# Performance work log

Hardware: AMD Instinct MI355X
Metric: run time of the kernel (lower is better)

## Reference

```python
import jax, jax.numpy as jnp
import numpy as np

NL, D, H, MLP, P, HW, L, KEEP = 6, 1024, 16, 4096, 16, 14, 196, 98
DH = D // H


def layer_norm(x, s, b):
    m = jnp.mean(x, axis=-1, keepdims=True)
    v = jnp.mean(jnp.square(x - m), axis=-1, keepdims=True)
    return (x - m) * jax.lax.rsqrt(v + 1e-6) * s + b


def gather_by_einsum(x, ids):
    # faithful to FLIP: one-hot gather expressed as matmul (sharding-friendly)
    mat = jax.nn.one_hot(ids, x.shape[1], dtype=x.dtype)
    return jnp.einsum('nl...,nkl->nk...', x, mat)


def setup_inputs():
    key = jax.random.key(0)
    ks = jax.random.split(key, 10)
    s = 0.02
    return {
        'imgs': jax.random.normal(ks[0], (32, 224, 224, 3), jnp.float32),
        'noise': jax.random.uniform(ks[1], (32, L), jnp.float32),
        'patch_w': jax.random.normal(ks[2], (P * P * 3, D), jnp.float32) * s,
        'patch_b': jnp.zeros((D,), jnp.float32),
        'pos_emb': jax.random.normal(ks[3], (1, L, D), jnp.float32) * s,
        'cls_token': jnp.zeros((1, 1, D), jnp.float32),
        'ln1_s': jnp.ones((NL, D), jnp.float32),
        'ln1_b': jnp.zeros((NL, D), jnp.float32),
        'wq': jax.random.normal(ks[4], (NL, D, D), jnp.float32) * s,
        'bq': jnp.zeros((NL, D), jnp.float32),
        'wk': jax.random.normal(ks[5], (NL, D, D), jnp.float32) * s,
        'bk': jnp.zeros((NL, D), jnp.float32),
        'wv': jax.random.normal(ks[6], (NL, D, D), jnp.float32) * s,
        'bv': jnp.zeros((NL, D), jnp.float32),
        'wo': jax.random.normal(ks[7], (NL, D, D), jnp.float32) * s,
        'bo': jnp.zeros((NL, D), jnp.float32),
        'ln2_s': jnp.ones((NL, D), jnp.float32),
        'ln2_b': jnp.zeros((NL, D), jnp.float32),
        'w1': jax.random.normal(ks[8], (NL, D, MLP), jnp.float32) * s,
        'b1': jnp.zeros((NL, MLP), jnp.float32),
        'w2': jax.random.normal(ks[9], (NL, MLP, D), jnp.float32) * s,
        'b2': jnp.zeros((NL, D), jnp.float32),
        'lnf_s': jnp.ones((D,), jnp.float32),
        'lnf_b': jnp.zeros((D,), jnp.float32),
    }


def reference(imgs, noise, patch_w, patch_b, pos_emb, cls_token,
              ln1_s, ln1_b, wq, bq, wk, bk, wv, bv, wo, bo,
              ln2_s, ln2_b, w1, b1, w2, b2, lnf_s, lnf_b):
    N = imgs.shape[0]
    # patchify: (N,224,224,3) -> (N, L=196, 768); stride-16 conv == patch matmul
    x = imgs.reshape(N, HW, P, HW, P, 3).transpose(0, 1, 3, 2, 4, 5).reshape(N, L, P * P * 3)
    x = x @ patch_w + patch_b          # (N, L, D)
    x = x + pos_emb

    # random_mask (mask_ratio=0.5 -> keep 98 of 196 tokens)
    ids_shuffle = jnp.argsort(noise, axis=1)
    ids_restore = jnp.argsort(ids_shuffle, axis=1)
    ids_keep = ids_shuffle[:, :KEEP]
    x = gather_by_einsum(x, ids_keep)  # (N, KEEP, D)
    mask = jnp.ones((N, L), x.dtype).at[:, :KEEP].set(0.0)
    mask = gather_by_einsum(mask, ids_restore)  # (N, L)

    # prepend cls token -> (N, 1+KEEP, D)
    x = jnp.concatenate([jnp.tile(cls_token, (N, 1, 1)), x], axis=1)

    scale = 1.0 / np.sqrt(DH).astype(np.float32)
    S = x.shape[1]
    for i in range(NL):
        y = layer_norm(x, ln1_s[i], ln1_b[i])
        q = (y @ wq[i] + bq[i]).reshape(N, S, H, DH)
        k = (y @ wk[i] + bk[i]).reshape(N, S, H, DH)
        v = (y @ wv[i] + bv[i]).reshape(N, S, H, DH)
        att = jax.nn.softmax(jnp.einsum('nqhd,nkhd->nhqk', q, k) * scale, axis=-1)
        o = jnp.einsum('nhqk,nkhd->nqhd', att, v).reshape(N, S, D)
        x = x + o @ wo[i] + bo[i]
        y = layer_norm(x, ln2_s[i], ln2_b[i])
        y = jax.nn.gelu(y @ w1[i] + b1[i]) @ w2[i] + b2[i]
        x = x + y
    x = layer_norm(x, lnf_s, lnf_b)
    return x, mask
```

## Files before the change

kernel.cpp:

```cpp
#include <hip/hip_runtime.h>
#include <hip/hip_bf16.h>
#include <math.h>

#define NLAYERS 6
#define DMODEL  1024
#define NHEADS  16
#define DHEAD   64
#define DMLP    4096
#define PSZ     16
#define HWN     14
#define LTOK    196
#define NKEEP   98
#define NIMG    32
#define SEQ     99
#define NS      (NIMG * SEQ)
#define NP      (NIMG * LTOK)
#define PDIM    768
#define QS      3072
#define SPAD    112
#define VT_PITCH 136
#define P_PITCH  136

typedef __attribute__((ext_vector_type(8))) short short8;
typedef __attribute__((ext_vector_type(4))) float f32x4;

__device__ __forceinline__ void gload16(const void* g, void* l) {
    __builtin_amdgcn_global_load_lds(
        (const __attribute__((address_space(1))) void*)g,
        (__attribute__((address_space(3))) void*)l, 16, 0, 0);
}

__global__ __launch_bounds__(256) void conv_transpose(
    const float* __restrict__ W, __hip_bfloat16* __restrict__ Wt, int K, int N,
    size_t src_zs, size_t dst_zs)
{
    __shared__ float tile[32][33];
    W += (size_t)blockIdx.z * src_zs;
    Wt += (size_t)blockIdx.z * dst_zs;
    int n0 = blockIdx.x * 32, k0 = blockIdx.y * 32;
    int tx = threadIdx.x & 31, ty = threadIdx.x >> 5;
#pragma unroll
    for (int i = 0; i < 4; ++i)
        tile[ty + i * 8][tx] = W[(size_t)(k0 + ty + i * 8) * N + n0 + tx];
    __syncthreads();
#pragma unroll
    for (int i = 0; i < 4; ++i)
        Wt[(size_t)(n0 + ty + i * 8) * K + k0 + tx] = __float2bfloat16(tile[tx][ty + i * 8]);
}

__global__ __launch_bounds__(256) void concat_bias(
    const float* __restrict__ bq, const float* __restrict__ bk,
    const float* __restrict__ bv, float* __restrict__ bqkv)
{
    int L = blockIdx.y;
    int i = blockIdx.x * 256 + threadIdx.x;
    float v;
    if (i < DMODEL)            v = bq[L * DMODEL + i];
    else if (i < 2 * DMODEL)   v = bk[L * DMODEL + i - DMODEL];
    else                       v = bv[L * DMODEL + i - 2 * DMODEL];
    bqkv[(size_t)L * QS + i] = v;
}

__global__ __launch_bounds__(256) void sort_kernel(
    const float* __restrict__ noise, int* __restrict__ ids_keep, float* __restrict__ mask)
{
    int n = blockIdx.x, tid = threadIdx.x;
    __shared__ float nz[LTOK];
    if (tid < LTOK) nz[tid] = noise[n * LTOK + tid];
    __syncthreads();
    if (tid < LTOK) {
        float val = nz[tid];
        int rank = 0;
        for (int j = 0; j < LTOK; ++j) {
            float vj = nz[j];
            rank += (vj < val) || (vj == val && j < tid);
        }
        mask[n * LTOK + tid] = (rank < NKEEP) ? 0.0f : 1.0f;
        if (rank < NKEEP) ids_keep[n * NKEEP + rank] = tid;
    }
}

__global__ __launch_bounds__(256) void patchify(
    const float* __restrict__ imgs, __hip_bfloat16* __restrict__ Ap)
{
    int row = blockIdx.x, tid = threadIdx.x;
    int n = row / LTOK, l = row % LTOK;
    int hy = l / HWN, hx = l % HWN;
    int py = tid >> 4, px = tid & 15;
    const float* src = imgs + (((size_t)(n * 224 + hy * 16 + py)) * 224 + hx * 16 + px) * 3;
    __hip_bfloat16* dst = Ap + (size_t)row * PDIM + tid * 3;
    dst[0] = __float2bfloat16(src[0]);
    dst[1] = __float2bfloat16(src[1]);
    dst[2] = __float2bfloat16(src[2]);
}

__global__ __launch_bounds__(256) void gather_cls(
    const float* __restrict__ x0, const float* __restrict__ cls,
    const int* __restrict__ ids_keep, float* __restrict__ x)
{
    int row = blockIdx.x, tid = threadIdx.x;
    int n = row / SEQ, s = row % SEQ;
    const float* src = (s == 0) ? cls
        : x0 + ((size_t)n * LTOK + ids_keep[n * NKEEP + (s - 1)]) * DMODEL;
    reinterpret_cast<float4*>(x + (size_t)row * DMODEL)[tid] =
        reinterpret_cast<const float4*>(src)[tid];
}

template <int OUTMODE>
__global__ __launch_bounds__(256) void ln_kernel(
    const float* __restrict__ x, const float* __restrict__ s, const float* __restrict__ b,
    float* __restrict__ of, __hip_bfloat16* __restrict__ ob)
{
    int row = blockIdx.x, tid = threadIdx.x;
    int lane = tid & 63, wid = tid >> 6;
    float4 t = reinterpret_cast<const float4*>(x + (size_t)row * DMODEL)[tid];
    float sum = t.x + t.y + t.z + t.w;
    float sq  = t.x * t.x + t.y * t.y + t.z * t.z + t.w * t.w;
#pragma unroll
    for (int m = 1; m < 64; m <<= 1) { sum += __shfl_xor(sum, m); sq += __shfl_xor(sq, m); }
    __shared__ float sm[8];
    if (lane == 0) { sm[wid] = sum; sm[4 + wid] = sq; }
    __syncthreads();
    sum = sm[0] + sm[1] + sm[2] + sm[3];
    sq  = sm[4] + sm[5] + sm[6] + sm[7];
    float mean = sum * (1.0f / DMODEL);
    float var  = sq * (1.0f / DMODEL) - mean * mean;
    float rstd = rsqrtf(var + 1e-6f);
    float4 sv = reinterpret_cast<const float4*>(s)[tid];
    float4 bv = reinterpret_cast<const float4*>(b)[tid];
    float o0 = (t.x - mean) * rstd * sv.x + bv.x;
    float o1 = (t.y - mean) * rstd * sv.y + bv.y;
    float o2 = (t.z - mean) * rstd * sv.z + bv.z;
    float o3 = (t.w - mean) * rstd * sv.w + bv.w;
    if (OUTMODE == 0) {
        reinterpret_cast<float4*>(of + (size_t)row * DMODEL)[tid] = make_float4(o0, o1, o2, o3);
    } else {
        __hip_bfloat16* p = ob + (size_t)row * DMODEL + tid * 4;
        p[0] = __float2bfloat16(o0); p[1] = __float2bfloat16(o1);
        p[2] = __float2bfloat16(o2); p[3] = __float2bfloat16(o3);
    }
}

template <int MODE>
__global__ __launch_bounds__(256) void gemm_mfma(
    const __hip_bfloat16* __restrict__ A, const __hip_bfloat16* __restrict__ Wt,
    const float* __restrict__ bias, const float* __restrict__ pos,
    float* __restrict__ Cf, __hip_bfloat16* __restrict__ Cb,
    int M, int N, int K)
{
    __shared__ __hip_bfloat16 As[2][128 * 32];
    __shared__ __hip_bfloat16 Bs[2][128 * 32];

    int tid = threadIdx.x;
    int lane = tid & 63, wid = tid >> 6;
    int quad = lane >> 4, l16 = lane & 15;
    int wm = wid & 1, wn = wid >> 1;
    int bm = blockIdx.x * 128, bn = blockIdx.y * 128;
    int Kc = K / gridDim.z;
    int koff = blockIdx.z * Kc;

    int rowA0 = tid >> 2,        rowA1 = (tid + 256) >> 2;
    int kcA0 = (tid & 3) ^ ((tid >> 3) & 3);
    int kcA1 = (tid & 3) ^ (((tid + 256) >> 3) & 3);
    int arow0 = bm + rowA0; if (arow0 >= M) arow0 = M - 1;
    int arow1 = bm + rowA1; if (arow1 >= M) arow1 = M - 1;
    const short* Ag0 = reinterpret_cast<const short*>(A) + (size_t)arow0 * K + koff + kcA0 * 8;
    const short* Ag1 = reinterpret_cast<const short*>(A) + (size_t)arow1 * K + koff + kcA1 * 8;
    const short* Bg0 = reinterpret_cast<const short*>(Wt) + (size_t)(bn + rowA0) * K + koff + kcA0 * 8;
    const short* Bg1 = reinterpret_cast<const short*>(Wt) + (size_t)(bn + rowA1) * K + koff + kcA1 * 8;

    int aOff[4], bOff[4];
#pragma unroll
    for (int t = 0; t < 4; ++t) {
        int row = wm * 64 + t * 16 + l16;
        aOff[t] = row * 64 + (quad ^ ((row >> 1) & 3)) * 16;
        int col = wn * 64 + t * 16 + l16;
        bOff[t] = col * 64 + (quad ^ ((col >> 1) & 3)) * 16;
    }

    f32x4 acc[4][4];
#pragma unroll
    for (int t = 0; t < 4; ++t)
#pragma unroll
        for (int u = 0; u < 4; ++u) { f32x4 z = {0.f, 0.f, 0.f, 0.f}; acc[t][u] = z; }

    auto stage = [&](int buf, int k0) {
        char* ad = (char*)As[buf];
        char* bd = (char*)Bs[buf];
        gload16(Ag0 + k0, ad + tid * 16);
        gload16(Ag1 + k0, ad + (tid + 256) * 16);
        gload16(Bg0 + k0, bd + tid * 16);
        gload16(Bg1 + k0, bd + (tid + 256) * 16);
    };
    auto compute = [&](int buf) {
        const char* ab = (const char*)As[buf];
        const char* bb = (const char*)Bs[buf];
        short8 a[4], b[4];
#pragma unroll
        for (int t = 0; t < 4; ++t) a[t] = *reinterpret_cast<const short8*>(ab + aOff[t]);
#pragma unroll
        for (int u = 0; u < 4; ++u) b[u] = *reinterpret_cast<const short8*>(bb + bOff[u]);
#pragma unroll
        for (int t = 0; t < 4; ++t)
#pragma unroll
            for (int u = 0; u < 4; ++u)
                acc[t][u] = __builtin_amdgcn_mfma_f32_16x16x32_bf16(a[t], b[u], acc[t][u], 0, 0, 0);
    };

    stage(0, 0);
    __syncthreads();
    for (int k0 = 0; k0 < Kc; k0 += 64) {
        stage(1, k0 + 32);
        compute(0);
        __syncthreads();
        if (k0 + 64 < Kc) stage(0, k0 + 64);
        compute(1);
        __syncthreads();
    }

    bool addb = (bias != nullptr) && (blockIdx.z == 0);
#pragma unroll
    for (int t = 0; t < 4; ++t) {
#pragma unroll
        for (int u = 0; u < 4; ++u) {
            int col = bn + wn * 64 + u * 16 + l16;
            float bcol = addb ? bias[col] : 0.0f;
#pragma unroll
            for (int i = 0; i < 4; ++i) {
                int row = bm + wm * 64 + t * 16 + quad * 4 + i;
                if (row >= M) continue;
                float val = acc[t][u][i] + bcol;
                size_t idx = (size_t)row * N + col;
                if (MODE == 0) {
                    if (pos) val += pos[(size_t)(row % LTOK) * N + col];
                    Cf[idx] = val;
                } else if (MODE == 1) {
                    atomicAdd(&Cf[idx], val);
                } else if (MODE == 2) {
                    float u3 = val * val * val;
                    float g = 0.5f * val *
                        (1.0f + tanhf(0.7978845608028654f * (val + 0.044715f * u3)));
                    Cb[idx] = __float2bfloat16(g);
                } else {
                    Cb[idx] = __float2bfloat16(val);
                }
            }
        }
    }
}

__global__ __launch_bounds__(256) void attn_mfma(
    const __hip_bfloat16* __restrict__ qkv, __hip_bfloat16* __restrict__ o)
{
    int n = blockIdx.x >> 4, h = blockIdx.x & 15;
    int tid = threadIdx.x, lane = tid & 63, wid = tid >> 6;
    int quad = lane >> 4, l16 = lane & 15;

    __shared__ __hip_bfloat16 Vt[DHEAD * VT_PITCH];
    __shared__ __hip_bfloat16 Ps[4][16 * P_PITCH];

    {
        int4 zz = make_int4(0, 0, 0, 0);
        int4* v4 = (int4*)Vt;
        int4* p4 = (int4*)Ps;
        for (int i = tid; i < (DHEAD * VT_PITCH) / 8; i += 256) v4[i] = zz;
        for (int i = tid; i < (4 * 16 * P_PITCH) / 8; i += 256) p4[i] = zz;
    }
    __syncthreads();
    for (int idx = tid; idx < SEQ * DHEAD; idx += 256) {
        int s = idx >> 6, d = idx & 63;
        Vt[d * VT_PITCH + s] = qkv[((size_t)(n * SEQ + s)) * QS + 2 * DMODEL + h * DHEAD + d];
    }
    __syncthreads();

    const short* qbase = reinterpret_cast<const short*>(qkv) + (size_t)n * SEQ * QS + h * DHEAD;
    const short* kbase = qbase + DMODEL;
    const float scale = 0.125f;

    for (int qt = wid; qt < 7; qt += 4) {
        int q0 = qt * 16;
        int qrow = q0 + l16; if (qrow >= SEQ) qrow = SEQ - 1;
        const short* qp = qbase + (size_t)qrow * QS + quad * 8;
        short8 aq0 = *reinterpret_cast<const short8*>(qp);
        short8 aq1 = *reinterpret_cast<const short8*>(qp + 32);

        f32x4 sc[7];
#pragma unroll
        for (int u = 0; u < 7; ++u) {
            int krow = u * 16 + l16; if (krow >= SEQ) krow = SEQ - 1;
            const short* kp = kbase + (size_t)krow * QS + quad * 8;
            short8 kb0 = *reinterpret_cast<const short8*>(kp);
            short8 kb1 = *reinterpret_cast<const short8*>(kp + 32);
            f32x4 s = {0.f, 0.f, 0.f, 0.f};
            s = __builtin_amdgcn_mfma_f32_16x16x32_bf16(aq0, kb0, s, 0, 0, 0);
            s = __builtin_amdgcn_mfma_f32_16x16x32_bf16(aq1, kb1, s, 0, 0, 0);
            sc[u] = s;
        }
#pragma unroll
        for (int u = 0; u < 7; ++u)
#pragma unroll
            for (int i = 0; i < 4; ++i)
                sc[u][i] *= scale;
        if (l16 >= 3) {
#pragma unroll
            for (int i = 0; i < 4; ++i) sc[6][i] = -1e30f;
        }
#pragma unroll
        for (int i = 0; i < 4; ++i) {
            float m = sc[0][i];
#pragma unroll
            for (int u = 1; u < 7; ++u) m = fmaxf(m, sc[u][i]);
            m = fmaxf(m, __shfl_xor(m, 1));
            m = fmaxf(m, __shfl_xor(m, 2));
            m = fmaxf(m, __shfl_xor(m, 4));
            m = fmaxf(m, __shfl_xor(m, 8));
            float sum = 0.f;
#pragma unroll
            for (int u = 0; u < 7; ++u) {
                float e = __expf(sc[u][i] - m);
                sc[u][i] = e;
                sum += e;
            }
            sum += __shfl_xor(sum, 1);
            sum += __shfl_xor(sum, 2);
            sum += __shfl_xor(sum, 4);
            sum += __shfl_xor(sum, 8);
            float inv = 1.0f / sum;
            __hip_bfloat16* pr = &Ps[wid][(quad * 4 + i) * P_PITCH];
#pragma unroll
            for (int u = 0; u < 7; ++u)
                pr[u * 16 + l16] = __float2bfloat16(sc[u][i] * inv);
        }
        short8 ap[4];
#pragma unroll
        for (int kc = 0; kc < 4; ++kc)
            ap[kc] = *reinterpret_cast<const short8*>(&Ps[wid][l16 * P_PITCH + kc * 32 + quad * 8]);
        f32x4 oacc[4];
#pragma unroll
        for (int dt = 0; dt < 4; ++dt) { f32x4 z = {0.f, 0.f, 0.f, 0.f}; oacc[dt] = z; }
#pragma unroll
        for (int kc = 0; kc < 4; ++kc) {
#pragma unroll
            for (int dt = 0; dt < 4; ++dt) {
                short8 vb = *reinterpret_cast<const short8*>(
                    &Vt[(dt * 16 + l16) * VT_PITCH + kc * 32 + quad * 8]);
                oacc[dt] = __builtin_amdgcn_mfma_f32_16x16x32_bf16(ap[kc], vb, oacc[dt], 0, 0, 0);
            }
        }
#pragma unroll
        for (int dt = 0; dt < 4; ++dt) {
#pragma unroll
            for (int i = 0; i < 4; ++i) {
                int row = q0 + quad * 4 + i;
                if (row < SEQ)
                    o[((size_t)(n * SEQ + row)) * DMODEL + h * DHEAD + dt * 16 + l16] =
                        __float2bfloat16(oacc[dt][i]);
            }
        }
    }
}

extern "C" void kernel_launch(void* const* d_in, const int* in_sizes, int n_in,
                              void* d_out, int out_size, void* d_ws, size_t ws_size,
                              hipStream_t stream)
{
    (void)in_sizes; (void)n_in; (void)out_size; (void)ws_size;
    const float* imgs    = (const float*)d_in[0];
    const float* noise   = (const float*)d_in[1];
    const float* patch_w = (const float*)d_in[2];
    const float* patch_b = (const float*)d_in[3];
    const float* pos_emb = (const float*)d_in[4];
    const float* cls     = (const float*)d_in[5];
    const float* ln1_s   = (const float*)d_in[6];
    const float* ln1_b   = (const float*)d_in[7];
    const float* wq      = (const float*)d_in[8];
    const float* bq      = (const float*)d_in[9];
    const float* wk      = (const float*)d_in[10];
    const float* bk      = (const float*)d_in[11];
    const float* wv      = (const float*)d_in[12];
    const float* bv      = (const float*)d_in[13];
    const float* wo      = (const float*)d_in[14];
    const float* bo      = (const float*)d_in[15];
    const float* ln2_s   = (const float*)d_in[16];
    const float* ln2_b   = (const float*)d_in[17];
    const float* w1      = (const float*)d_in[18];
    const float* b1      = (const float*)d_in[19];
    const float* w2      = (const float*)d_in[20];
    const float* b2      = (const float*)d_in[21];
    const float* lnf_s   = (const float*)d_in[22];
    const float* lnf_b   = (const float*)d_in[23];

    float* out_x    = (float*)d_out;
    float* out_mask = out_x + (size_t)NS * DMODEL;

    char* p = (char*)d_ws;
    auto alloc = [&](size_t bytes) {
        char* r = p; p += (bytes + 255) & ~(size_t)255; return r;
    };
    __hip_bfloat16* patch_wt = (__hip_bfloat16*)alloc((size_t)DMODEL * PDIM * 2);
    __hip_bfloat16* wqkvt    = (__hip_bfloat16*)alloc((size_t)NLAYERS * QS * DMODEL * 2);
    __hip_bfloat16* wot = (__hip_bfloat16*)alloc((size_t)NLAYERS * DMODEL * DMODEL * 2);
    __hip_bfloat16* w1t = (__hip_bfloat16*)alloc((size_t)NLAYERS * DMODEL * DMLP * 2);
    __hip_bfloat16* w2t = (__hip_bfloat16*)alloc((size_t)NLAYERS * DMODEL * DMLP * 2);
    float* bqkv     = (float*)alloc((size_t)NLAYERS * QS * 4);
    int*   ids_keep = (int*)alloc((size_t)NIMG * NKEEP * 4);
    float* x        = (float*)alloc((size_t)NS * DMODEL * 4);
    char* scratch = p;
    __hip_bfloat16* ybf  = (__hip_bfloat16*)alloc((size_t)NS * DMODEL * 2);
    __hip_bfloat16* qkv  = (__hip_bfloat16*)alloc((size_t)NS * QS * 2);
    __hip_bfloat16* obf  = (__hip_bfloat16*)alloc((size_t)NS * DMODEL * 2);
    __hip_bfloat16* h1bf = (__hip_bfloat16*)alloc((size_t)NS * DMLP * 2);
    __hip_bfloat16* Apatch = (__hip_bfloat16*)scratch;
    float* x0 = (float*)(scratch + (((size_t)NP * PDIM * 2 + 255) & ~(size_t)255));

    const size_t DD = (size_t)DMODEL * DMODEL;
    const size_t DM = (size_t)DMODEL * DMLP;

    conv_transpose<<<dim3(DMODEL / 32, PDIM / 32, 1), 256, 0, stream>>>(
        patch_w, patch_wt, PDIM, DMODEL, PDIM * DMODEL, PDIM * DMODEL);
    conv_transpose<<<dim3(DMODEL / 32, DMODEL / 32, NLAYERS), 256, 0, stream>>>(
        wq, wqkvt, DMODEL, DMODEL, DD, (size_t)QS * DMODEL);
    conv_transpose<<<dim3(DMODEL / 32, DMODEL / 32, NLAYERS), 256, 0, stream>>>(
        wk, wqkvt + DD, DMODEL, DMODEL, DD, (size_t)QS * DMODEL);
    conv_transpose<<<dim3(DMODEL / 32, DMODEL / 32, NLAYERS), 256, 0, stream>>>(
        wv, wqkvt + 2 * DD, DMODEL, DMODEL, DD, (size_t)QS * DMODEL);
    conv_transpose<<<dim3(DMODEL / 32, DMODEL / 32, NLAYERS), 256, 0, stream>>>(
        wo, wot, DMODEL, DMODEL, DD, DD);
    conv_transpose<<<dim3(DMLP / 32, DMODEL / 32, NLAYERS), 256, 0, stream>>>(
        w1, w1t, DMODEL, DMLP, DM, DM);
    conv_transpose<<<dim3(DMODEL / 32, DMLP / 32, NLAYERS), 256, 0, stream>>>(
        w2, w2t, DMLP, DMODEL, DM, DM);
    concat_bias<<<dim3(QS / 256, NLAYERS), 256, 0, stream>>>(bq, bk, bv, bqkv);

    sort_kernel<<<NIMG, 256, 0, stream>>>(noise, ids_keep, out_mask);
    patchify<<<NP, 256, 0, stream>>>(imgs, Apatch);
    gemm_mfma<0><<<dim3(NP / 128, DMODEL / 128), 256, 0, stream>>>(
        Apatch, patch_wt, patch_b, pos_emb, x0, nullptr, NP, DMODEL, PDIM);
    gather_cls<<<NS, 256, 0, stream>>>(x0, cls, ids_keep, x);

    dim3 gQKV((NS + 127) / 128, QS / 128);
    dim3 gD((NS + 127) / 128, DMODEL / 128);
    dim3 gM((NS + 127) / 128, DMLP / 128);
    dim3 gWo((NS + 127) / 128, DMODEL / 128, 2);
    dim3 gW2((NS + 127) / 128, DMODEL / 128, 4);
    for (int L = 0; L < NLAYERS; ++L) {
        size_t wDD = (size_t)L * DD;
        size_t wDM = (size_t)L * DM;
        ln_kernel<1><<<NS, 256, 0, stream>>>(x, ln1_s + L * DMODEL, ln1_b + L * DMODEL, nullptr, ybf);
        gemm_mfma<3><<<gQKV, 256, 0, stream>>>(ybf, wqkvt + (size_t)L * QS * DMODEL,
                                               bqkv + (size_t)L * QS, nullptr, nullptr, qkv,
                                               NS, QS, DMODEL);
        attn_mfma<<<NIMG * NHEADS, 256, 0, stream>>>(qkv, obf);
        gemm_mfma<1><<<gWo, 256, 0, stream>>>(obf, wot + wDD, bo + L * DMODEL, nullptr, x, nullptr, NS, DMODEL, DMODEL);
        ln_kernel<1><<<NS, 256, 0, stream>>>(x, ln2_s + L * DMODEL, ln2_b + L * DMODEL, nullptr, ybf);
        gemm_mfma<2><<<gM, 256, 0, stream>>>(ybf, w1t + wDM, b1 + L * DMLP, nullptr, nullptr, h1bf, NS, DMLP, DMODEL);
        gemm_mfma<1><<<gW2, 256, 0, stream>>>(h1bf, w2t + wDM, b2 + L * DMODEL, nullptr, x, nullptr, NS, DMODEL, DMLP);
    }

    ln_kernel<0><<<NS, 256, 0, stream>>>(x, lnf_s, lnf_b, out_x, nullptr);
}
```

Before: 2.266 ms.

## Triple-buffer GEMM pipeline, remap blocks per XCD, fuse split-K reduction into layernorm

The GEMM moves from a double-buffered LDS loop to a three-stage ring. It uses explicit vmcnt waits and a single barrier per step so that global loads overlap more compute. Workgroup IDs are remapped so neighbouring tiles land on the same XCD. The Wo and W2 split-K GEMMs now write partial sums to a workspace instead of using atomicAdd, and the following layernorm sums the partials, bias and residual and writes x back. This removes float atomics and gives a deterministic reduction, at the cost of more LDS, extra partial-buffer traffic, and a fallback path for when the workspace is too small.

Measured after the change: 2.037 ms. 1.11x faster.

```diff
diff --git a/kernel.cpp b/kernel.cpp
--- a/kernel.cpp
+++ b/kernel.cpp
@@ -106,14 +106,26 @@
         reinterpret_cast<const float4*>(src)[tid];
 }
 
-template <int OUTMODE>
+template <int OUTMODE, int NPART>
 __global__ __launch_bounds__(256) void ln_kernel(
-    const float* __restrict__ x, const float* __restrict__ s, const float* __restrict__ b,
+    const float* __restrict__ x, float* __restrict__ xw,
+    const float* __restrict__ part, const float* __restrict__ rb,
+    const float* __restrict__ s, const float* __restrict__ b,
     float* __restrict__ of, __hip_bfloat16* __restrict__ ob)
 {
     int row = blockIdx.x, tid = threadIdx.x;
     int lane = tid & 63, wid = tid >> 6;
     float4 t = reinterpret_cast<const float4*>(x + (size_t)row * DMODEL)[tid];
+    if (NPART == 2) {
+        float4 a0 = reinterpret_cast<const float4*>(part + (size_t)row * DMODEL)[tid];
+        float4 a1 = reinterpret_cast<const float4*>(part + (size_t)(NS + row) * DMODEL)[tid];
+        float4 rv = reinterpret_cast<const float4*>(rb)[tid];
+        t.x += a0.x + a1.x + rv.x;
+        t.y += a0.y + a1.y + rv.y;
+        t.z += a0.z + a1.z + rv.z;
+        t.w += a0.w + a1.w + rv.w;
+        reinterpret_cast<float4*>(xw + (size_t)row * DMODEL)[tid] = t;
+    }
     float sum = t.x + t.y + t.z + t.w;
     float sq  = t.x * t.x + t.y * t.y + t.z * t.z + t.w * t.w;
 #pragma unroll
@@ -148,16 +160,25 @@
     float* __restrict__ Cf, __hip_bfloat16* __restrict__ Cb,
     int M, int N, int K)
 {
-    __shared__ __hip_bfloat16 As[2][128 * 32];
-    __shared__ __hip_bfloat16 Bs[2][128 * 32];
+    __shared__ __hip_bfloat16 As[3][128 * 32];
+    __shared__ __hip_bfloat16 Bs[3][128 * 32];
+
+    int nwg = gridDim.x * gridDim.y * gridDim.z;
+    int orig = (blockIdx.z * gridDim.y + blockIdx.y) * gridDim.x + blockIdx.x;
+    int q = nwg >> 3, r = nwg & 7, xcd = orig & 7, lin = orig >> 3;
+    int wg = (xcd < r ? xcd * (q + 1) : r * (q + 1) + (xcd - r) * q) + lin;
+    int bx = wg % gridDim.x;
+    int tmp = wg / gridDim.x;
+    int by = tmp % gridDim.y;
+    int bz = tmp / gridDim.y;
 
     int tid = threadIdx.x;
     int lane = tid & 63, wid = tid >> 6;
     int quad = lane >> 4, l16 = lane & 15;
     int wm = wid & 1, wn = wid >> 1;
-    int bm = blockIdx.x * 128, bn = blockIdx.y * 128;
+    int bm = bx * 128, bn = by * 128;
     int Kc = K / gridDim.z;
-    int koff = blockIdx.z * Kc;
+    int koff = bz * Kc;
 
     int rowA0 = tid >> 2,        rowA1 = (tid + 256) >> 2;
     int kcA0 = (tid & 3) ^ ((tid >> 3) & 3);
@@ -207,42 +228,53 @@
                 acc[t][u] = __builtin_amdgcn_mfma_f32_16x16x32_bf16(a[t], b[u], acc[t][u], 0, 0, 0);
     };
 
+    const int nsteps = Kc >> 5;
     stage(0, 0);
-    __syncthreads();
-    for (int k0 = 0; k0 < Kc; k0 += 64) {
-        stage(1, k0 + 32);
-        compute(0);
-        __syncthreads();
-        if (k0 + 64 < Kc) stage(0, k0 + 64);
-        compute(1);
-        __syncthreads();
-    }
-
-    bool addb = (bias != nullptr) && (blockIdx.z == 0);
-#pragma unroll
-    for (int t = 0; t < 4; ++t) {
+    stage(1, 32);
+    int kst = 64;
+    int t = 0;
+
+#define PIPE_ITER(B) { \
+        if (t == nsteps - 1) { asm volatile("s_waitcnt vmcnt(0)" ::: "memory"); } \
+        else                 { asm volatile("s_waitcnt vmcnt(4)" ::: "memory"); } \
+        __builtin_amdgcn_s_barrier(); \
+        __builtin_amdgcn_sched_barrier(0); \
+        if (kst < Kc) { stage(((B) + 2) % 3, kst); kst += 32; } \
+        compute(B); \
+        ++t; }
+
+    while (t + 3 <= nsteps) { PIPE_ITER(0) PIPE_ITER(1) PIPE_ITER(2) }
+    if (t < nsteps) { PIPE_ITER(0) }
+    if (t < nsteps) { PIPE_ITER(1) }
+#undef PIPE_ITER
+
+    bool addb = (bias != nullptr) && (bz == 0);
+#pragma unroll
+    for (int t2 = 0; t2 < 4; ++t2) {
 #pragma unroll
         for (int u = 0; u < 4; ++u) {
             int col = bn + wn * 64 + u * 16 + l16;
             float bcol = addb ? bias[col] : 0.0f;
 #pragma unroll
             for (int i = 0; i < 4; ++i) {
-                int row = bm + wm * 64 + t * 16 + quad * 4 + i;
+                int row = bm + wm * 64 + t2 * 16 + quad * 4 + i;
                 if (row >= M) continue;
-                float val = acc[t][u][i] + bcol;
+                float val = acc[t2][u][i] + bcol;
                 size_t idx = (size_t)row * N + col;
                 if (MODE == 0) {
                     if (pos) val += pos[(size_t)(row % LTOK) * N + col];
                     Cf[idx] = val;
                 } else if (MODE == 1) {
-                    atomicAdd(&Cf[idx], val);
+                    Cf[idx] += val;
                 } else if (MODE == 2) {
                     float u3 = val * val * val;
                     float g = 0.5f * val *
                         (1.0f + tanhf(0.7978845608028654f * (val + 0.044715f * u3)));
                     Cb[idx] = __float2bfloat16(g);
+                } else if (MODE == 3) {
+                    Cb[idx] = __float2bfloat16(val);
                 } else {
-                    Cb[idx] = __float2bfloat16(val);
+                    Cf[(size_t)bz * ((size_t)M * N) + idx] = val;
                 }
             }
         }
@@ -364,7 +396,7 @@
                               void* d_out, int out_size, void* d_ws, size_t ws_size,
                               hipStream_t stream)
 {
-    (void)in_sizes; (void)n_in; (void)out_size; (void)ws_size;
+    (void)in_sizes; (void)n_in; (void)out_size;
     const float* imgs    = (const float*)d_in[0];
     const float* noise   = (const float*)d_in[1];
     const float* patch_w = (const float*)d_in[2];
@@ -412,6 +444,8 @@
     __hip_bfloat16* h1bf = (__hip_bfloat16*)alloc((size_t)NS * DMLP * 2);
     __hip_bfloat16* Apatch = (__hip_bfloat16*)scratch;
     float* x0 = (float*)(scratch + (((size_t)NP * PDIM * 2 + 255) & ~(size_t)255));
+    float* partial = (float*)alloc((size_t)2 * NS * DMODEL * 4);
+    bool useSK = (size_t)(p - (char*)d_ws) <= ws_size;
 
     const size_t DD = (size_t)DMODEL * DMODEL;
     const size_t DM = (size_t)DMODEL * DMLP;
@@ -441,21 +475,46 @@
     dim3 gQKV((NS + 127) / 128, QS / 128);
     dim3 gD((NS + 127) / 128, DMODEL / 128);
     dim3 gM((NS + 127) / 128, DMLP / 128);
-    dim3 gWo((NS + 127) / 128, DMODEL / 128, 2);
-    dim3 gW2((NS + 127) / 128, DMODEL / 128, 4);
+    dim3 gSK((NS + 127) / 128, DMODEL / 128, 2);
     for (int L = 0; L < NLAYERS; ++L) {
         size_t wDD = (size_t)L * DD;
         size_t wDM = (size_t)L * DM;
-        ln_kernel<1><<<NS, 256, 0, stream>>>(x, ln1_s + L * DMODEL, ln1_b + L * DMODEL, nullptr, ybf);
+        if (L == 0 || !useSK)
+            ln_kernel<1, 0><<<NS, 256, 0, stream>>>(x, nullptr, nullptr, nullptr,
+                ln1_s + L * DMODEL, ln1_b + L * DMODEL, nullptr, ybf);
+        else
+            ln_kernel<1, 2><<<NS, 256, 0, stream>>>(x, x, partial, b2 + (size_t)(L - 1) * DMODEL,
+                ln1_s + L * DMODEL, ln1_b + L * DMODEL, nullptr, ybf);
         gemm_mfma<3><<<gQKV, 256, 0, stream>>>(ybf, wqkvt + (size_t)L * QS * DMODEL,
                                                bqkv + (size_t)L * QS, nullptr, nullptr, qkv,
                                                NS, QS, DMODEL);
         attn_mfma<<<NIMG * NHEADS, 256, 0, stream>>>(qkv, obf);
-        gemm_mfma<1><<<gWo, 256, 0, stream>>>(obf, wot + wDD, bo + L * DMODEL, nullptr, x, nullptr, NS, DMODEL, DMODEL);
-        ln_kernel<1><<<NS, 256, 0, stream>>>(x, ln2_s + L * DMODEL, ln2_b + L * DMODEL, nullptr, ybf);
-        gemm_mfma<2><<<gM, 256, 0, stream>>>(ybf, w1t + wDM, b1 + L * DMLP, nullptr, nullptr, h1bf, NS, DMLP, DMODEL);
-        gemm_mfma<1><<<gW2, 256, 0, stream>>>(h1bf, w2t + wDM, b2 + L * DMODEL, nullptr, x, nullptr, NS, DMODEL, DMLP);
-    }
-
-    ln_kernel<0><<<NS, 256, 0, stream>>>(x, lnf_s, lnf_b, out_x, nullptr);
-}
+        if (useSK) {
+            gemm_mfma<4><<<gSK, 256, 0, stream>>>(obf, wot + wDD, nullptr, nullptr,
+                                                  partial, nullptr, NS, DMODEL, DMODEL);
+            ln_kernel<1, 2><<<NS, 256, 0, stream>>>(x, x, partial, bo + (size_t)L * DMODEL,
+                ln2_s + L * DMODEL, ln2_b + L * DMODEL, nullptr, ybf);
+        } else {
+            gemm_mfma<1><<<gD, 256, 0, stream>>>(obf, wot + wDD, bo + L * DMODEL, nullptr,
+                                                 x, nullptr, NS, DMODEL, DMODEL);
+            ln_kernel<1, 0><<<NS, 256, 0, stream>>>(x, nullptr, nullptr, nullptr,
+                ln2_s + L * DMODEL, ln2_b + L * DMODEL, nullptr, ybf);
+        }
+        gemm_mfma<2><<<gM, 256, 0, stream>>>(ybf, w1t + wDM, b1 + L * DMLP, nullptr,
+                                             nullptr, h1bf, NS, DMLP, DMODEL);
+        if (useSK) {
+            gemm_mfma<4><<<gSK, 256, 0, stream>>>(h1bf, w2t + wDM, nullptr, nullptr,
+                                                  partial, nullptr, NS, DMODEL, DMLP);
+        } else {
+            gemm_mfma<1><<<gD, 256, 0, stream>>>(h1bf, w2t + wDM, b2 + L * DMODEL, nullptr,
+                                                 x, nullptr, NS, DMODEL, DMLP);
+        }
+    }
+
+    if (useSK)
+        ln_kernel<0, 2><<<NS, 256, 0, stream>>>(x, x, partial, b2 + (size_t)5 * DMODEL,
+                                                lnf_s, lnf_b, out_x, nullptr);
+    else
+        ln_kernel<0, 0><<<NS, 256, 0, stream>>>(x, nullptr, nullptr, nullptr,
+                                                lnf_s, lnf_b, out_x, nullptr);
+}
```
